# Kernel optimization log

Hardware: AMD Instinct MI355X
Metric: run time of the kernel (lower is better)

The kernel has to match this reference:

```python
import jax, jax.numpy as jnp
import numpy as np

N, E, G, D, C = 50000, 800000, 512, 128, 10
BN_EPS = 1e-5

def setup_inputs() -> dict:
    key = jax.random.key(0)
    ks = jax.random.split(key, 12)
    inp = {
        'x': jnp.zeros((N,), dtype=jnp.int64 if jax.config.jax_enable_x64 else jnp.int32),
        'edge_index': jax.random.randint(ks[0], (2, E), 0, N),
        'batch_ids': jnp.sort(jax.random.randint(ks[1], (N,), 0, G)),
        'emb': jax.random.normal(ks[2], (1, D), jnp.float32),
        'W1a': jax.random.normal(ks[3], (D, D), jnp.float32) * 0.05,
        'b1a': jnp.zeros((D,), jnp.float32),
        'g1': jnp.ones((D,), jnp.float32),
        'be1': jnp.zeros((D,), jnp.float32),
        'W1b': jax.random.normal(ks[4], (D, D), jnp.float32) * 0.05,
        'b1b': jnp.zeros((D,), jnp.float32),
        'W2a': jax.random.normal(ks[5], (D, D), jnp.float32) * 0.05,
        'b2a': jnp.zeros((D,), jnp.float32),
        'g2': jnp.ones((D,), jnp.float32),
        'be2': jnp.zeros((D,), jnp.float32),
        'W2b': jax.random.normal(ks[6], (D, D), jnp.float32) * 0.05,
        'b2b': jnp.zeros((D,), jnp.float32),
        'Wm': jax.random.normal(ks[7], (D, C), jnp.float32) * 0.05,
        'bm': jnp.zeros((C,), jnp.float32),
        'Wx': jax.random.normal(ks[8], (D, C), jnp.float32) * 0.05,
        'bx': jnp.zeros((C,), jnp.float32),
        'ens_w': jnp.array([0.6, 0.4], jnp.float32),
    }
    return inp

def _gin_layer(h, src, dst, Wa, ba, g, be, Wb, bb):
    # GINConv, eps=0: mlp(x + sum_{j in N(i)} x_j)
    agg = jax.ops.segment_sum(h[src], dst, num_segments=N)  # [N, D]
    z = (h + agg) @ Wa + ba
    mu = jnp.mean(z, axis=0)
    var = jnp.var(z, axis=0)  # biased, as torch BN training forward
    z = (z - mu) * jax.lax.rsqrt(var + BN_EPS) * g + be
    z = jax.nn.relu(z)  # dropout is identity in eval
    return z @ Wb + bb

def reference(x, edge_index, batch_ids, emb, W1a, b1a, g1, be1, W1b, b1b,
              W2a, b2a, g2, be2, W2b, b2b, Wm, bm, Wx, bx, ens_w):
    src, dst = edge_index[0], edge_index[1]
    h0 = emb[x]  # [N, D] (all indices 0)
    h1 = _gin_layer(h0, src, dst, W1a, b1a, g1, be1, W1b, b1b)
    h2 = _gin_layer(h1, src, dst, W2a, b2a, g2, be2, W2b, b2b) + h1
    # global mean / max pooling over batch segments
    counts = jax.ops.segment_sum(jnp.ones((N,), h2.dtype), batch_ids, num_segments=G)
    mean_repr = jax.ops.segment_sum(h2, batch_ids, num_segments=G) / jnp.maximum(counts, 1.0)[:, None]
    max_repr = jax.ops.segment_max(h2, batch_ids, num_segments=G)
    max_repr = jnp.where(jnp.isfinite(max_repr), max_repr, 0.0)  # empty segments -> 0
    logits_mean = mean_repr @ Wm + bm
    logits_max = max_repr @ Wx + bx
    w = jax.nn.softmax(ens_w)
    ensemble_logits = w[0] * logits_mean + w[1] * logits_max
    return (ensemble_logits, logits_mean, logits_max, (mean_repr, max_repr))
```

## Files before the change

kernel.cpp:

```cpp
#include <hip/hip_runtime.h>
#include <math.h>

#define N_NODES  50000
#define N_EDGES  800000
#define N_GRAPHS 512
#define DIM      128
#define NCLS     10
#define KH       64
#define KW       32
#define KT       128
#define OVF_CAP  65536
#define BN_EPS   1e-5f

#define NB_GEMM  ((N_NODES + 63) / 64)
#define NB_DEG   ((N_NODES + 255) / 256)


__global__ void k_zero(uint4* __restrict__ p, long long n4) {
    long long i = (long long)blockIdx.x * blockDim.x + threadIdx.x;
    if (i < n4) p[i] = make_uint4(0u, 0u, 0u, 0u);
}

__global__ void k_count_deg(const int* __restrict__ dst, int* __restrict__ deg) {
    int e = blockIdx.x * blockDim.x + threadIdx.x;
    if (e < N_EDGES) atomicAdd(&deg[dst[e]], 1);
}

__global__ void k_sumdeg2(const int* __restrict__ deg, unsigned long long* __restrict__ dpart) {
    __shared__ unsigned long long lds[256];
    int i = blockIdx.x * blockDim.x + threadIdx.x;
    unsigned long long v = 0;
    if (i < N_NODES) {
        unsigned long long d = (unsigned long long)(unsigned int)deg[i];
        v = d * d;
    }
    lds[threadIdx.x] = v;
    __syncthreads();
    for (int s = blockDim.x >> 1; s > 0; s >>= 1) {
        if ((int)threadIdx.x < s) lds[threadIdx.x] += lds[threadIdx.x + s];
        __syncthreads();
    }
    if (threadIdx.x == 0) dpart[blockIdx.x] = lds[0];
}

__device__ inline int lower_bound_i(const int* __restrict__ a, int n, int v) {
    int lo = 0, hi = n;
    while (lo < hi) {
        int mid = (lo + hi) >> 1;
        if (a[mid] < v) lo = mid + 1; else hi = mid;
    }
    return lo;
}

__global__ void k_bounds(const int* __restrict__ batch, int* __restrict__ seg) {
    int g = threadIdx.x;
    if (g < N_GRAPHS) seg[g] = lower_bound_i(batch, N_NODES, g);
    if (g == 0) seg[N_GRAPHS] = N_NODES;
}

__global__ void k_prep(const float* __restrict__ emb, const float* __restrict__ W1a,
                       const float* __restrict__ g1, const float* __restrict__ be1,
                       const unsigned long long* __restrict__ dpart,
                       float* __restrict__ A, float* __restrict__ B) {
    int d = threadIdx.x;
    float u = 0.f;
    for (int k = 0; k < DIM; ++k) u += emb[k] * W1a[k * DIM + d];
    unsigned long long s2 = 0;
    #pragma unroll 4
    for (int b = 0; b < NB_DEG; ++b) s2 += dpart[b];
    double mdeg = (double)N_EDGES / (double)N_NODES;
    double vdeg = (double)s2 / (double)N_NODES - mdeg * mdeg;
    float var = (float)((double)u * (double)u * vdeg);
    float rs  = rsqrtf(var + BN_EPS);
    float a   = u * rs * g1[d];
    A[d] = a;
    B[d] = be1[d] - (float)mdeg * a;
}

__global__ void k_tables(const float* __restrict__ A, const float* __restrict__ B,
                         const float* __restrict__ W1b, const float* __restrict__ b1b,
                         const float* __restrict__ W2a,
                         float* __restrict__ table, float* __restrict__ table2) {
    int k = blockIdx.x, d = threadIdx.x;
    __shared__ float r[DIM];
    __shared__ float t[DIM];
    float kf = (float)k;
    r[d] = fmaxf(kf * A[d] + B[d], 0.f);
    __syncthreads();
    float acc = b1b[d];
    for (int j = 0; j < DIM; ++j) acc += r[j] * W1b[j * DIM + d];
    table[(size_t)k * DIM + d] = acc;
    t[d] = acc;
    __syncthreads();
    float acc2 = 0.f;
    for (int j = 0; j < DIM; ++j) acc2 += t[j] * W2a[j * DIM + d];
    table2[(size_t)k * DIM + d] = acc2;
}

__global__ void k_edges(const int* __restrict__ src, const int* __restrict__ dst,
                        const int* __restrict__ deg, unsigned int* __restrict__ m,
                        unsigned int* __restrict__ ovf_cnt, int* __restrict__ ovf_buf) {
    int e = blockIdx.x * blockDim.x + threadIdx.x;
    if (e >= N_EDGES) return;
    int s = src[e], dd = dst[e];
    int k = deg[s];
    if (k < KH) {
        atomicAdd(&m[(size_t)dd * KW + (k >> 1)], 1u << ((k & 1) << 4));
    } else {
        unsigned int idx = atomicAdd(ovf_cnt, 1u);
        if (idx < OVF_CAP) {
            ovf_buf[2 * idx] = dd;
            ovf_buf[2 * idx + 1] = k;
        }
    }
}

__global__ __launch_bounds__(256) void k_gemm1(
        const unsigned int* __restrict__ m, const int* __restrict__ deg,
        const float* __restrict__ table2, const float* __restrict__ b2a,
        float* __restrict__ z2, float* __restrict__ spart,
        const unsigned int* __restrict__ ovf_cnt, const int* __restrict__ ovf_buf) {
    __shared__ __align__(16) float lds_t2[64 * 128];
    __shared__ __align__(16) unsigned int lds_m[64 * 33];
    const int t = threadIdx.x;
    const int i0 = blockIdx.x * 64;
    #pragma unroll
    for (int q = 0; q < 8; ++q) {
        int idx = t + 256 * q;
        int row = idx >> 5, c = (idx & 31) << 2;
        *(float4*)&lds_t2[row * 128 + c] = *(const float4*)&table2[(size_t)row * 128 + c];
    }
    #pragma unroll
    for (int q = 0; q < 2; ++q) {
        int idx = t + 256 * q;
        int row = idx >> 3, c = (idx & 7) << 2;
        uint4 v = make_uint4(0u, 0u, 0u, 0u);
        if (i0 + row < N_NODES) v = *(const uint4*)&m[(size_t)(i0 + row) * KW + c];
        lds_m[row * 33 + c + 0] = v.x;
        lds_m[row * 33 + c + 1] = v.y;
        lds_m[row * 33 + c + 2] = v.z;
        lds_m[row * 33 + c + 3] = v.w;
    }
    __syncthreads();

    const int g = t >> 5;
    const int c4 = (t & 31) << 2;
    const int rbase = g * 8;
    float acc[8][4] = {};
    #pragma unroll 4
    for (int w = 0; w < KW; ++w) {
        float4 ta = *(const float4*)&lds_t2[(2 * w) * 128 + c4];
        float4 tb = *(const float4*)&lds_t2[(2 * w + 1) * 128 + c4];
        #pragma unroll
        for (int r = 0; r < 8; ++r) {
            unsigned int mw = lds_m[(rbase + r) * 33 + w];
            float lo = (float)(mw & 0xFFFFu);
            float hi = (float)(mw >> 16);
            acc[r][0] += lo * ta.x + hi * tb.x;
            acc[r][1] += lo * ta.y + hi * tb.y;
            acc[r][2] += lo * ta.z + hi * tb.z;
            acc[r][3] += lo * ta.w + hi * tb.w;
        }
    }

    unsigned int nov = *ovf_cnt;
    if (nov > OVF_CAP) nov = OVF_CAP;
    for (unsigned int u = 0; u < nov; ++u) {
        int dd = ovf_buf[2 * u];
        int r = dd - i0;
        if (r >= 0 && r < 64 && (r >> 3) == g) {
            int kk = ovf_buf[2 * u + 1]; if (kk > KT - 1) kk = KT - 1;
            float4 tv = *(const float4*)&table2[(size_t)kk * DIM + c4];
            acc[r & 7][0] += tv.x; acc[r & 7][1] += tv.y;
            acc[r & 7][2] += tv.z; acc[r & 7][3] += tv.w;
        }
    }

    float4 bb = *(const float4*)&b2a[c4];
    float s4[4] = {0.f, 0.f, 0.f, 0.f};
    float q4[4] = {0.f, 0.f, 0.f, 0.f};
    #pragma unroll
    for (int r = 0; r < 8; ++r) {
        int row = i0 + rbase + r;
        if (row < N_NODES) {
            int kk = deg[row];
            float4 self;
            if (kk < KH) self = *(const float4*)&lds_t2[kk * 128 + c4];
            else {
                if (kk > KT - 1) kk = KT - 1;
                self = *(const float4*)&table2[(size_t)kk * DIM + c4];
            }
            float v0 = acc[r][0] + self.x + bb.x;
            float v1 = acc[r][1] + self.y + bb.y;
            float v2 = acc[r][2] + self.z + bb.z;
            float v3 = acc[r][3] + self.w + bb.w;
            *(float4*)&z2[(size_t)row * DIM + c4] = make_float4(v0, v1, v2, v3);
            s4[0] += v0; q4[0] += v0 * v0;
            s4[1] += v1; q4[1] += v1 * v1;
            s4[2] += v2; q4[2] += v2 * v2;
            s4[3] += v3; q4[3] += v3 * v3;
        }
    }
    __syncthreads();
    float* red = (float*)lds_m;
    #pragma unroll
    for (int j = 0; j < 4; ++j) {
        red[g * 128 + c4 + j] = s4[j];
        red[1024 + g * 128 + c4 + j] = q4[j];
    }
    __syncthreads();
    if (t < 128) {
        float ss = 0.f, qq = 0.f;
        #pragma unroll
        for (int gg = 0; gg < 8; ++gg) {
            ss += red[gg * 128 + t];
            qq += red[1024 + gg * 128 + t];
        }
        spart[(size_t)blockIdx.x * 256 + t] = ss;
        spart[(size_t)blockIdx.x * 256 + 128 + t] = qq;
    }
}

__global__ __launch_bounds__(1024) void k_fin2(
        const float* __restrict__ spart,
        const float* __restrict__ g2, const float* __restrict__ be2,
        float* __restrict__ A2, float* __restrict__ B2) {
    __shared__ double red[4 * 256];
    int t = threadIdx.x & 255;
    int q = threadIdx.x >> 8;
    double acc = 0.0;
    #pragma unroll 4
    for (int b = q; b < NB_GEMM; b += 4) acc += (double)spart[(size_t)b * 256 + t];
    red[q * 256 + t] = acc;
    __syncthreads();
    if (threadIdx.x < 256)
        red[threadIdx.x] = red[threadIdx.x] + red[256 + threadIdx.x] +
                           red[512 + threadIdx.x] + red[768 + threadIdx.x];
    __syncthreads();
    if (threadIdx.x < 128) {
        double mu = red[threadIdx.x] / (double)N_NODES;
        double var = red[128 + threadIdx.x] / (double)N_NODES - mu * mu;
        float rs = rsqrtf((float)var + BN_EPS);
        float a = rs * g2[threadIdx.x];
        A2[threadIdx.x] = a;
        B2[threadIdx.x] = be2[threadIdx.x] - (float)mu * a;
    }
}

__global__ __launch_bounds__(256) void k_gemm2(
        const float* __restrict__ z2, const float* __restrict__ A2, const float* __restrict__ B2,
        const float* __restrict__ W2b, const float* __restrict__ b2b,
        const float* __restrict__ table, const int* __restrict__ deg,
        float* __restrict__ h2) {
    __shared__ __align__(16) float lds_zn[64 * 132];
    const int t = threadIdx.x;
    const int i0 = blockIdx.x * 64;
    #pragma unroll
    for (int q = 0; q < 8; ++q) {
        int idx = t + 256 * q;
        int row = idx >> 5, cc = (idx & 31) << 2;
        float4 zv = make_float4(0.f, 0.f, 0.f, 0.f);
        if (i0 + row < N_NODES) zv = *(const float4*)&z2[(size_t)(i0 + row) * DIM + cc];
        float4 av = *(const float4*)&A2[cc];
        float4 bv = *(const float4*)&B2[cc];
        lds_zn[row * 132 + cc + 0] = fmaxf(zv.x * av.x + bv.x, 0.f);
        lds_zn[row * 132 + cc + 1] = fmaxf(zv.y * av.y + bv.y, 0.f);
        lds_zn[row * 132 + cc + 2] = fmaxf(zv.z * av.z + bv.z, 0.f);
        lds_zn[row * 132 + cc + 3] = fmaxf(zv.w * av.w + bv.w, 0.f);
    }
    __syncthreads();

    const int g = t >> 5;
    const int c4 = (t & 31) << 2;
    const int rbase = g * 8;
    float acc[8][4] = {};
    float4 wa[4], wb[4];
    #pragma unroll
    for (int j = 0; j < 4; ++j)
        wa[j] = *(const float4*)&W2b[(size_t)j * DIM + c4];
    #pragma unroll 2
    for (int kb = 0; kb < 32; ++kb) {
        const float4* cur = (kb & 1) ? wb : wa;
        float4* nxt = (kb & 1) ? wa : wb;
        if (kb < 31) {
            #pragma unroll
            for (int j = 0; j < 4; ++j)
                nxt[j] = *(const float4*)&W2b[(size_t)((kb + 1) * 4 + j) * DIM + c4];
        }
        #pragma unroll
        for (int j = 0; j < 4; ++j) {
            int k = kb * 4 + j;
            float4 wv = cur[j];
            #pragma unroll
            for (int r = 0; r < 8; ++r) {
                float zv = lds_zn[(rbase + r) * 132 + k];
                acc[r][0] += zv * wv.x;
                acc[r][1] += zv * wv.y;
                acc[r][2] += zv * wv.z;
                acc[r][3] += zv * wv.w;
            }
        }
    }

    float4 bbv = *(const float4*)&b2b[c4];
    #pragma unroll
    for (int r = 0; r < 8; ++r) {
        int row = i0 + rbase + r;
        if (row < N_NODES) {
            int kk = deg[row]; if (kk > KT - 1) kk = KT - 1;
            float4 tb = *(const float4*)&table[(size_t)kk * DIM + c4];
            float4 o;
            o.x = acc[r][0] + bbv.x + tb.x;
            o.y = acc[r][1] + bbv.y + tb.y;
            o.z = acc[r][2] + bbv.z + tb.z;
            o.w = acc[r][3] + bbv.w + tb.w;
            *(float4*)&h2[(size_t)row * DIM + c4] = o;
        }
    }
}

__global__ __launch_bounds__(1024) void k_pool(
        const float* __restrict__ h2, const int* __restrict__ seg,
        float* __restrict__ out_mean, float* __restrict__ out_max) {
    __shared__ float reds[32 * 132];
    __shared__ float redm[32 * 132];
    int g = blockIdx.x;
    int s0 = seg[g], e0 = seg[g + 1];
    int rg = threadIdx.x >> 5;
    int c4 = (threadIdx.x & 31) << 2;
    float s[4] = {0.f, 0.f, 0.f, 0.f};
    float mx[4] = {-INFINITY, -INFINITY, -INFINITY, -INFINITY};
    for (int i = s0 + rg; i < e0; i += 32) {
        float4 v = *(const float4*)&h2[(size_t)i * DIM + c4];
        s[0] += v.x; mx[0] = fmaxf(mx[0], v.x);
        s[1] += v.y; mx[1] = fmaxf(mx[1], v.y);
        s[2] += v.z; mx[2] = fmaxf(mx[2], v.z);
        s[3] += v.w; mx[3] = fmaxf(mx[3], v.w);
    }
    #pragma unroll
    for (int j = 0; j < 4; ++j) {
        reds[rg * 132 + c4 + j] = s[j];
        redm[rg * 132 + c4 + j] = mx[j];
    }
    __syncthreads();
    for (int step = 16; step >= 1; step >>= 1) {
        if (rg < step) {
            #pragma unroll
            for (int j = 0; j < 4; ++j) {
                reds[rg * 132 + c4 + j] += reds[(rg + step) * 132 + c4 + j];
                redm[rg * 132 + c4 + j] = fmaxf(redm[rg * 132 + c4 + j],
                                                redm[(rg + step) * 132 + c4 + j]);
            }
        }
        __syncthreads();
    }
    if (rg == 0) {
        int cnt = e0 - s0;
        float denom = (float)(cnt > 0 ? cnt : 1);
        #pragma unroll
        for (int j = 0; j < 4; ++j) {
            float sum = reds[c4 + j];
            float mxv = redm[c4 + j];
            out_mean[(size_t)g * DIM + c4 + j] = sum / denom;
            out_max[(size_t)g * DIM + c4 + j]  = (cnt > 0) ? mxv : 0.f;
        }
    }
}

__global__ void k_head(const float* __restrict__ mean_repr, const float* __restrict__ max_repr,
                       const float* __restrict__ Wm, const float* __restrict__ bm,
                       const float* __restrict__ Wx, const float* __restrict__ bx,
                       const float* __restrict__ ensw,
                       float* __restrict__ out_ens, float* __restrict__ out_lm,
                       float* __restrict__ out_lx) {
    int g = blockIdx.x, c = threadIdx.x;
    if (c >= NCLS) return;
    float lm = bm[c], lx = bx[c];
    const float* mr = mean_repr + (size_t)g * DIM;
    const float* xr = max_repr + (size_t)g * DIM;
    for (int d = 0; d < DIM; ++d) {
        lm += mr[d] * Wm[d * NCLS + c];
        lx += xr[d] * Wx[d * NCLS + c];
    }
    float a0 = ensw[0], a1 = ensw[1];
    float mw = fmaxf(a0, a1);
    float e0 = expf(a0 - mw), e1 = expf(a1 - mw);
    float inv = 1.f / (e0 + e1);
    float w0 = e0 * inv, w1 = e1 * inv;
    out_lm[(size_t)g * NCLS + c] = lm;
    out_lx[(size_t)g * NCLS + c] = lx;
    out_ens[(size_t)g * NCLS + c] = w0 * lm + w1 * lx;
}


extern "C" void kernel_launch(void* const* d_in, const int* in_sizes, int n_in,
                              void* d_out, int out_size, void* d_ws, size_t ws_size,
                              hipStream_t stream) {
    const int* edge = (const int*)d_in[1];
    const int* src = edge;
    const int* dst = edge + N_EDGES;
    const int* batch = (const int*)d_in[2];
    const float* emb = (const float*)d_in[3];
    const float* W1a = (const float*)d_in[4];
    const float* g1  = (const float*)d_in[6];
    const float* be1 = (const float*)d_in[7];
    const float* W1b = (const float*)d_in[8];
    const float* b1b = (const float*)d_in[9];
    const float* W2a = (const float*)d_in[10];
    const float* b2a = (const float*)d_in[11];
    const float* g2  = (const float*)d_in[12];
    const float* be2 = (const float*)d_in[13];
    const float* W2b = (const float*)d_in[14];
    const float* b2b = (const float*)d_in[15];
    const float* Wm  = (const float*)d_in[16];
    const float* bm  = (const float*)d_in[17];
    const float* Wx  = (const float*)d_in[18];
    const float* bx  = (const float*)d_in[19];
    const float* ensw = (const float*)d_in[20];

    char* ws = (char*)d_ws;
    size_t off = 0;
    auto take = [&](size_t bytes) {
        char* p = ws + off;
        off += (bytes + 511) & ~(size_t)511;
        return p;
    };
    int* deg                  = (int*)take((size_t)N_NODES * 4);
    unsigned int* m           = (unsigned int*)take((size_t)N_NODES * KW * 4);
    unsigned int* ovf_cnt     = (unsigned int*)take(4);
    size_t zbytes = off;
    unsigned long long* dpart = (unsigned long long*)take((size_t)NB_DEG * 8);
    float* spart              = (float*)take((size_t)NB_GEMM * 256 * 4);
    int* ovf_buf              = (int*)take((size_t)OVF_CAP * 2 * 4);
    float* table              = (float*)take((size_t)KT * DIM * 4);
    float* table2             = (float*)take((size_t)KT * DIM * 4);
    float* A                  = (float*)take(DIM * 4);
    float* B                  = (float*)take(DIM * 4);
    float* A2                 = (float*)take(DIM * 4);
    float* B2                 = (float*)take(DIM * 4);
    int* seg                  = (int*)take((size_t)(N_GRAPHS + 1) * 4);
    float* z2                 = (float*)take((size_t)N_NODES * DIM * 4);
    float* h2                 = (float*)take((size_t)N_NODES * DIM * 4);
    (void)ws_size; (void)in_sizes; (void)n_in; (void)out_size;

    float* out      = (float*)d_out;
    float* out_ens  = out;
    float* out_lm   = out + (size_t)N_GRAPHS * NCLS;
    float* out_lx   = out + 2 * (size_t)N_GRAPHS * NCLS;
    float* out_mean = out + 3 * (size_t)N_GRAPHS * NCLS;
    float* out_max  = out_mean + (size_t)N_GRAPHS * DIM;

    long long n4 = (long long)(zbytes >> 4);
    k_zero<<<(int)((n4 + 255) / 256), 256, 0, stream>>>((uint4*)ws, n4);
    k_count_deg<<<(N_EDGES + 255) / 256, 256, 0, stream>>>(dst, deg);
    k_bounds<<<1, N_GRAPHS, 0, stream>>>(batch, seg);
    k_sumdeg2<<<NB_DEG, 256, 0, stream>>>(deg, dpart);
    k_prep<<<1, DIM, 0, stream>>>(emb, W1a, g1, be1, dpart, A, B);
    k_tables<<<KT, DIM, 0, stream>>>(A, B, W1b, b1b, W2a, table, table2);
    k_edges<<<(N_EDGES + 255) / 256, 256, 0, stream>>>(src, dst, deg, m, ovf_cnt, ovf_buf);
    k_gemm1<<<NB_GEMM, 256, 0, stream>>>(m, deg, table2, b2a, z2, spart, ovf_cnt, ovf_buf);
    k_fin2<<<1, 1024, 0, stream>>>(spart, g2, be2, A2, B2);
    k_gemm2<<<NB_GEMM, 256, 0, stream>>>(z2, A2, B2, W2b, b2b, table, deg, h2);
    k_pool<<<N_GRAPHS, 1024, 0, stream>>>(h2, seg, out_mean, out_max);
    k_head<<<N_GRAPHS, 64, 0, stream>>>(out_mean, out_max, Wm, bm, Wx, bx, ensw,
                                        out_ens, out_lm, out_lx);
}
```

Measured before the change: 201.4 us.

## Merge small prep kernels, fuse pooling with head, vectorize gemm2 LDS reads

Folds the k_bounds, k_sumdeg2 and k_prep kernels into a single 512-thread block that does the binary searches, the degree-squared reduction and the BN1 coefficients. It also fuses the logits head into the pooling kernel, and moves k_edges ahead of the prep kernel. In gemm2, the inner loop now reads four LDS values at once as a float4 and drops the double-buffered weight prefetch. The goal is fewer launches and fewer LDS instructions. In exchange, the degree reduction now runs in one block over 50k entries, which is serial work, and the weight loads are no longer prefetched.

```diff
diff --git a/kernel.cpp b/kernel.cpp
--- a/kernel.cpp
+++ b/kernel.cpp
@@ -13,7 +13,6 @@
 #define BN_EPS   1e-5f
 
 #define NB_GEMM  ((N_NODES + 63) / 64)
-#define NB_DEG   ((N_NODES + 255) / 256)
 
 
 __global__ void k_zero(uint4* __restrict__ p, long long n4) {
@@ -24,23 +23,6 @@
 __global__ void k_count_deg(const int* __restrict__ dst, int* __restrict__ deg) {
     int e = blockIdx.x * blockDim.x + threadIdx.x;
     if (e < N_EDGES) atomicAdd(&deg[dst[e]], 1);
-}
-
-__global__ void k_sumdeg2(const int* __restrict__ deg, unsigned long long* __restrict__ dpart) {
-    __shared__ unsigned long long lds[256];
-    int i = blockIdx.x * blockDim.x + threadIdx.x;
-    unsigned long long v = 0;
-    if (i < N_NODES) {
-        unsigned long long d = (unsigned long long)(unsigned int)deg[i];
-        v = d * d;
-    }
-    lds[threadIdx.x] = v;
-    __syncthreads();
-    for (int s = blockDim.x >> 1; s > 0; s >>= 1) {
-        if ((int)threadIdx.x < s) lds[threadIdx.x] += lds[threadIdx.x + s];
-        __syncthreads();
-    }
-    if (threadIdx.x == 0) dpart[blockIdx.x] = lds[0];
 }
 
 __device__ inline int lower_bound_i(const int* __restrict__ a, int n, int v) {
@@ -52,29 +34,38 @@
     return lo;
 }
 
-__global__ void k_bounds(const int* __restrict__ batch, int* __restrict__ seg) {
-    int g = threadIdx.x;
-    if (g < N_GRAPHS) seg[g] = lower_bound_i(batch, N_NODES, g);
-    if (g == 0) seg[N_GRAPHS] = N_NODES;
-}
-
-__global__ void k_prep(const float* __restrict__ emb, const float* __restrict__ W1a,
-                       const float* __restrict__ g1, const float* __restrict__ be1,
-                       const unsigned long long* __restrict__ dpart,
-                       float* __restrict__ A, float* __restrict__ B) {
-    int d = threadIdx.x;
-    float u = 0.f;
-    for (int k = 0; k < DIM; ++k) u += emb[k] * W1a[k * DIM + d];
-    unsigned long long s2 = 0;
-    #pragma unroll 4
-    for (int b = 0; b < NB_DEG; ++b) s2 += dpart[b];
-    double mdeg = (double)N_EDGES / (double)N_NODES;
-    double vdeg = (double)s2 / (double)N_NODES - mdeg * mdeg;
-    float var = (float)((double)u * (double)u * vdeg);
-    float rs  = rsqrtf(var + BN_EPS);
-    float a   = u * rs * g1[d];
-    A[d] = a;
-    B[d] = be1[d] - (float)mdeg * a;
+__global__ __launch_bounds__(512) void k_prep2(
+        const int* __restrict__ batch, int* __restrict__ seg,
+        const int* __restrict__ deg,
+        const float* __restrict__ emb, const float* __restrict__ W1a,
+        const float* __restrict__ g1, const float* __restrict__ be1,
+        float* __restrict__ A, float* __restrict__ B) {
+    __shared__ unsigned long long sred[512];
+    const int t = threadIdx.x;
+    seg[t] = lower_bound_i(batch, N_NODES, t);
+    if (t == 0) seg[N_GRAPHS] = N_NODES;
+    unsigned long long s = 0;
+    for (int i = t; i < N_NODES; i += 512) {
+        unsigned long long d = (unsigned long long)(unsigned int)deg[i];
+        s += d * d;
+    }
+    sred[t] = s;
+    __syncthreads();
+    for (int st = 256; st > 0; st >>= 1) {
+        if (t < st) sred[t] += sred[t + st];
+        __syncthreads();
+    }
+    if (t < DIM) {
+        float u = 0.f;
+        for (int k = 0; k < DIM; ++k) u += emb[k] * W1a[k * DIM + t];
+        double mdeg = (double)N_EDGES / (double)N_NODES;
+        double vdeg = (double)sred[0] / (double)N_NODES - mdeg * mdeg;
+        float var = (float)((double)u * (double)u * vdeg);
+        float rs  = rsqrtf(var + BN_EPS);
+        float a   = u * rs * g1[t];
+        A[t] = a;
+        B[t] = be1[t] - (float)mdeg * a;
+    }
 }
 
 __global__ void k_tables(const float* __restrict__ A, const float* __restrict__ B,
@@ -274,31 +265,20 @@
     const int c4 = (t & 31) << 2;
     const int rbase = g * 8;
     float acc[8][4] = {};
-    float4 wa[4], wb[4];
-    #pragma unroll
-    for (int j = 0; j < 4; ++j)
-        wa[j] = *(const float4*)&W2b[(size_t)j * DIM + c4];
     #pragma unroll 2
     for (int kb = 0; kb < 32; ++kb) {
-        const float4* cur = (kb & 1) ? wb : wa;
-        float4* nxt = (kb & 1) ? wa : wb;
-        if (kb < 31) {
-            #pragma unroll
-            for (int j = 0; j < 4; ++j)
-                nxt[j] = *(const float4*)&W2b[(size_t)((kb + 1) * 4 + j) * DIM + c4];
-        }
+        const int k0 = kb * 4;
+        float4 w0 = *(const float4*)&W2b[(size_t)(k0 + 0) * DIM + c4];
+        float4 w1 = *(const float4*)&W2b[(size_t)(k0 + 1) * DIM + c4];
+        float4 w2 = *(const float4*)&W2b[(size_t)(k0 + 2) * DIM + c4];
+        float4 w3 = *(const float4*)&W2b[(size_t)(k0 + 3) * DIM + c4];
         #pragma unroll
-        for (int j = 0; j < 4; ++j) {
-            int k = kb * 4 + j;
-            float4 wv = cur[j];
-            #pragma unroll
-            for (int r = 0; r < 8; ++r) {
-                float zv = lds_zn[(rbase + r) * 132 + k];
-                acc[r][0] += zv * wv.x;
-                acc[r][1] += zv * wv.y;
-                acc[r][2] += zv * wv.z;
-                acc[r][3] += zv * wv.w;
-            }
+        for (int r = 0; r < 8; ++r) {
+            float4 zr = *(const float4*)&lds_zn[(rbase + r) * 132 + k0];
+            acc[r][0] += zr.x * w0.x + zr.y * w1.x + zr.z * w2.x + zr.w * w3.x;
+            acc[r][1] += zr.x * w0.y + zr.y * w1.y + zr.z * w2.y + zr.w * w3.y;
+            acc[r][2] += zr.x * w0.z + zr.y * w1.z + zr.z * w2.z + zr.w * w3.z;
+            acc[r][3] += zr.x * w0.w + zr.y * w1.w + zr.z * w2.w + zr.w * w3.w;
         }
     }
 
@@ -319,8 +299,13 @@
     }
 }
 
-__global__ __launch_bounds__(1024) void k_pool(
+__global__ __launch_bounds__(1024) void k_poolhead(
         const float* __restrict__ h2, const int* __restrict__ seg,
+        const float* __restrict__ Wm, const float* __restrict__ bm,
+        const float* __restrict__ Wx, const float* __restrict__ bx,
+        const float* __restrict__ ensw,
+        float* __restrict__ out_ens, float* __restrict__ out_lm,
+        float* __restrict__ out_lx,
         float* __restrict__ out_mean, float* __restrict__ out_max) {
     __shared__ float reds[32 * 132];
     __shared__ float redm[32 * 132];
@@ -359,37 +344,30 @@
         float denom = (float)(cnt > 0 ? cnt : 1);
         #pragma unroll
         for (int j = 0; j < 4; ++j) {
-            float sum = reds[c4 + j];
-            float mxv = redm[c4 + j];
-            out_mean[(size_t)g * DIM + c4 + j] = sum / denom;
-            out_max[(size_t)g * DIM + c4 + j]  = (cnt > 0) ? mxv : 0.f;
-        }
-    }
-}
-
-__global__ void k_head(const float* __restrict__ mean_repr, const float* __restrict__ max_repr,
-                       const float* __restrict__ Wm, const float* __restrict__ bm,
-                       const float* __restrict__ Wx, const float* __restrict__ bx,
-                       const float* __restrict__ ensw,
-                       float* __restrict__ out_ens, float* __restrict__ out_lm,
-                       float* __restrict__ out_lx) {
-    int g = blockIdx.x, c = threadIdx.x;
-    if (c >= NCLS) return;
-    float lm = bm[c], lx = bx[c];
-    const float* mr = mean_repr + (size_t)g * DIM;
-    const float* xr = max_repr + (size_t)g * DIM;
-    for (int d = 0; d < DIM; ++d) {
-        lm += mr[d] * Wm[d * NCLS + c];
-        lx += xr[d] * Wx[d * NCLS + c];
-    }
-    float a0 = ensw[0], a1 = ensw[1];
-    float mw = fmaxf(a0, a1);
-    float e0 = expf(a0 - mw), e1 = expf(a1 - mw);
-    float inv = 1.f / (e0 + e1);
-    float w0 = e0 * inv, w1 = e1 * inv;
-    out_lm[(size_t)g * NCLS + c] = lm;
-    out_lx[(size_t)g * NCLS + c] = lx;
-    out_ens[(size_t)g * NCLS + c] = w0 * lm + w1 * lx;
+            float mean = reds[c4 + j] / denom;
+            float mxv  = (cnt > 0) ? redm[c4 + j] : 0.f;
+            out_mean[(size_t)g * DIM + c4 + j] = mean;
+            out_max[(size_t)g * DIM + c4 + j]  = mxv;
+            reds[c4 + j] = mean;
+            redm[c4 + j] = mxv;
+        }
+    }
+    __syncthreads();
+    int t = threadIdx.x;
+    if (t < NCLS) {
+        float lm = bm[t], lx = bx[t];
+        for (int d = 0; d < DIM; ++d) {
+            lm += reds[d] * Wm[d * NCLS + t];
+            lx += redm[d] * Wx[d * NCLS + t];
+        }
+        float a0 = ensw[0], a1 = ensw[1];
+        float mw = fmaxf(a0, a1);
+        float e0v = expf(a0 - mw), e1v = expf(a1 - mw);
+        float inv = 1.f / (e0v + e1v);
+        out_lm[(size_t)g * NCLS + t] = lm;
+        out_lx[(size_t)g * NCLS + t] = lx;
+        out_ens[(size_t)g * NCLS + t] = (e0v * inv) * lm + (e1v * inv) * lx;
+    }
 }
 
 
@@ -429,7 +407,6 @@
     unsigned int* m           = (unsigned int*)take((size_t)N_NODES * KW * 4);
     unsigned int* ovf_cnt     = (unsigned int*)take(4);
     size_t zbytes = off;
-    unsigned long long* dpart = (unsigned long long*)take((size_t)NB_DEG * 8);
     float* spart              = (float*)take((size_t)NB_GEMM * 256 * 4);
     int* ovf_buf              = (int*)take((size_t)OVF_CAP * 2 * 4);
     float* table              = (float*)take((size_t)KT * DIM * 4);
@@ -453,15 +430,12 @@
     long long n4 = (long long)(zbytes >> 4);
     k_zero<<<(int)((n4 + 255) / 256), 256, 0, stream>>>((uint4*)ws, n4);
     k_count_deg<<<(N_EDGES + 255) / 256, 256, 0, stream>>>(dst, deg);
-    k_bounds<<<1, N_GRAPHS, 0, stream>>>(batch, seg);
-    k_sumdeg2<<<NB_DEG, 256, 0, stream>>>(deg, dpart);
-    k_prep<<<1, DIM, 0, stream>>>(emb, W1a, g1, be1, dpart, A, B);
+    k_edges<<<(N_EDGES + 255) / 256, 256, 0, stream>>>(src, dst, deg, m, ovf_cnt, ovf_buf);
+    k_prep2<<<1, 512, 0, stream>>>(batch, seg, deg, emb, W1a, g1, be1, A, B);
     k_tables<<<KT, DIM, 0, stream>>>(A, B, W1b, b1b, W2a, table, table2);
-    k_edges<<<(N_EDGES + 255) / 256, 256, 0, stream>>>(src, dst, deg, m, ovf_cnt, ovf_buf);
     k_gemm1<<<NB_GEMM, 256, 0, stream>>>(m, deg, table2, b2a, z2, spart, ovf_cnt, ovf_buf);
     k_fin2<<<1, 1024, 0, stream>>>(spart, g2, be2, A2, B2);
     k_gemm2<<<NB_GEMM, 256, 0, stream>>>(z2, A2, B2, W2b, b2b, table, deg, h2);
-    k_pool<<<N_GRAPHS, 1024, 0, stream>>>(h2, seg, out_mean, out_max);
-    k_head<<<N_GRAPHS, 64, 0, stream>>>(out_mean, out_max, Wm, bm, Wx, bx, ensw,
-                                        out_ens, out_lm, out_lx);
-}
+    k_poolhead<<<N_GRAPHS, 1024, 0, stream>>>(h2, seg, Wm, bm, Wx, bx, ensw,
+                                              out_ens, out_lm, out_lx, out_mean, out_max);
+}
```

Result: no change. 201.5 us (+0.0%).
